# Optimization experiments

Measured on AMD Instinct MI355X. Metric: run time of the kernel, lower is better.

The kernel has to match this reference:

```python
import jax, jax.numpy as jnp
import numpy as np

C = 1024        # number of classes
N = 8           # proxies per class
ALLNUM = C * N  # 8192 total proxies
DIM = 512
R = 0.05
TOPK = int(np.ceil(R * ALLNUM))  # 410
LAM = 0.3
B = 2048


def setup_inputs() -> dict:
    key = jax.random.key(0)
    k1, k2, k3 = jax.random.split(key, 3)
    inp = jax.random.normal(k1, (B, DIM), dtype=jnp.float32)
    target = jax.random.randint(k2, (B,), 0, C, dtype=jnp.int64)
    # kaiming-uniform-initialized proxies approximated by scaled normal init
    proxies = jax.random.normal(k3, (DIM, ALLNUM), dtype=jnp.float32)
    instance_label = jnp.repeat(jnp.arange(C, dtype=jnp.int64), N)  # [ALLNUM]
    return {"input": inp, "target": target, "Proxies": proxies,
            "instance_label": instance_label}


def reference(input, target, Proxies, instance_label):
    # L2-normalize each proxy column (F.normalize along dim=0, eps=1e-12)
    norm = jnp.maximum(jnp.linalg.norm(Proxies, axis=0, keepdims=True), 1e-12)
    centers = Proxies / norm                             # [DIM, ALLNUM]
    similarity = input @ centers                          # [B, ALLNUM]

    positive_mask = (target[:, None] == instance_label[None, :]).astype(similarity.dtype)
    _, indices = jax.lax.top_k(similarity + 1000.0 * positive_mask, TOPK)  # [B, TOPK]

    rows = jnp.arange(similarity.shape[0])[:, None]
    mask = jnp.zeros_like(similarity).at[rows, indices].set(1.0)
    prob_a = mask * similarity                            # sparse-masked similarities

    y_instance_onehot = jax.nn.one_hot(instance_label, C, dtype=similarity.dtype)  # [ALLNUM, C]
    logits = prob_a @ y_instance_onehot                   # [B, C]

    y_target_onehot = jax.nn.one_hot(target, C, dtype=similarity.dtype)  # [B, C]
    logits_mask = 1.0 - (logits == 0.0).astype(similarity.dtype)

    # scale_mask_softmax with scale=1 along dim=1
    e = jnp.exp(logits) * logits_mask
    predict = e / (1e-8 + jnp.sum(e, axis=1, keepdims=True))
    lossClassify = jnp.mean(jnp.sum(-y_target_onehot * jnp.log(predict + 1e-20), axis=1))

    # proxy regularizer: cross-entropy of proxy-vs-class logits
    simCenter = centers.T @ centers                       # [ALLNUM, ALLNUM]
    centers_logits = simCenter @ y_instance_onehot        # [ALLNUM, C]
    logp = jax.nn.log_softmax(centers_logits, axis=1)
    reg = -jnp.mean(jnp.take_along_axis(logp, instance_label[:, None], axis=1))

    return (lossClassify + LAM * reg, lossClassify)
```

## Files before the change

### kernel.cpp

```cpp
#include <hip/hip_runtime.h>
#include <hip/hip_bf16.h>
#include <math.h>

#define C_CLS   1024
#define NPROXY  8
#define ALLNUM  8192
#define DIM     512
#define TOPK    410
#define LAM     0.3f
#define BATCH   2048

#define BAND_CAP_BLK 40
#define ROW_CAP      512
#define GCAP         64

typedef __bf16 bf16x8 __attribute__((ext_vector_type(8)));
typedef float floatx4 __attribute__((ext_vector_type(4)));
typedef unsigned short ushort_t;

#define WS_RNORM 0
#define WS_SIG   8192
#define WS_LP    10240
#define WS_RP    12288
#define WS_CNT   14336
#define WS_NDEF  16384
#define WS_FLAG  18432
#define WS_CLS   20480
#define WS_BVAL  (WS_CLS + 2048*1024)
#define WS_BCOL  (WS_BVAL + 2048*512)
#define WS_ABF   (WS_BCOL + 2048*256)
#define WS_PBF   (WS_ABF + 524288)
#define WS_STBF  (WS_PBF + 2097152)
#define WS_MX    (WS_STBF + 262144)
#define WS_SE    (WS_MX + 65536)
#define WS_DIAG  (WS_SE + 65536)
#define WS_SYNC  (WS_DIAG + 8192)

__device__ inline float block_reduce(float v, int is_max, float* red, int t) {
    #pragma unroll
    for (int o = 32; o > 0; o >>= 1) {
        float w = __shfl_down(v, o);
        v = is_max ? fmaxf(v, w) : (v + w);
    }
    __syncthreads();
    if ((t & 63) == 0) red[t >> 6] = v;
    __syncthreads();
    float r = is_max ? fmaxf(fmaxf(red[0], red[1]), fmaxf(red[2], red[3]))
                     : (red[0] + red[1] + red[2] + red[3]);
    __syncthreads();
    return r;
}

__device__ inline ushort_t f2bf(float f) {
    unsigned u = __float_as_uint(f);
    return (ushort_t)((u + 0x7FFFu + ((u >> 16) & 1u)) >> 16);
}

__device__ inline float bf2f(ushort_t u) {
    return __uint_as_float(((unsigned)u) << 16);
}

__device__ inline void ld_g2l_16(const void* g, void* l) {
    __builtin_amdgcn_global_load_lds(
        (const __attribute__((address_space(1))) unsigned int*)g,
        (__attribute__((address_space(3))) unsigned int*)l,
        16, 0, 0);
}

__device__ inline unsigned f2ord(float f) {
    unsigned u = __float_as_uint(f);
    return (u & 0x80000000u) ? ~u : (u | 0x80000000u);
}

__global__ __launch_bounds__(256) void k_prep1(const float* __restrict__ P,
                                               const float* __restrict__ input,
                                               float* __restrict__ rnorm,
                                               float* __restrict__ rowsig,
                                               ushort_t* __restrict__ Abf,
                                               ushort_t* __restrict__ Pbf,
                                               ushort_t* __restrict__ Stbf,
                                               unsigned* __restrict__ zaux,
                                               unsigned* __restrict__ zsync) {
    __shared__ float stile[512 * 17];
    __shared__ float cred[256];
    __shared__ float s_rn[16];
    int bx = blockIdx.x, t = threadIdx.x;
    if (bx < 512) {
        int c0 = bx * 16;
        #pragma unroll
        for (int it = 0; it < 8; ++it) {
            int r = it * 64 + (t >> 2);
            int c4 = (t & 3) * 4;
            float4 v = *(const float4*)&P[(size_t)r * ALLNUM + c0 + c4];
            stile[r * 17 + c4]     = v.x;
            stile[r * 17 + c4 + 1] = v.y;
            stile[r * 17 + c4 + 2] = v.z;
            stile[r * 17 + c4 + 3] = v.w;
        }
        __syncthreads();
        int tc = t & 15, g = t >> 4;
        float s = 0.f;
        #pragma unroll 8
        for (int k = 0; k < 32; ++k) {
            float v = stile[(g * 32 + k) * 17 + tc];
            s += v * v;
        }
        cred[g * 16 + tc] = s;
        __syncthreads();
        if (g == 0) {
            float tot = 0.f;
            #pragma unroll
            for (int k = 0; k < 16; ++k) tot += cred[k * 16 + tc];
            float r = 1.0f / fmaxf(sqrtf(tot), 1e-12f);
            rnorm[c0 + tc] = r;
            s_rn[tc] = r;
        }
        __syncthreads();
        #pragma unroll
        for (int p = 0; p < 8; ++p) {
            int idx = t + 256 * p;
            int c = idx >> 7, d4 = (idx & 127) * 4;
            ushort4 o;
            o.x = f2bf(stile[(d4    ) * 17 + c]);
            o.y = f2bf(stile[(d4 + 1) * 17 + c]);
            o.z = f2bf(stile[(d4 + 2) * 17 + c]);
            o.w = f2bf(stile[(d4 + 3) * 17 + c]);
            *(ushort4*)&Pbf[(size_t)(c0 + c) * DIM + d4] = o;
        }
        #pragma unroll
        for (int p = 0; p < 2; ++p) {
            int idx = t + 256 * p;
            int cc = idx >> 8, d2 = (idx & 255) * 2;
            float v0 = 0.f, v1 = 0.f;
            #pragma unroll
            for (int n = 0; n < 8; ++n) {
                float rr = s_rn[cc * 8 + n];
                v0 += stile[(d2    ) * 17 + cc * 8 + n] * rr;
                v1 += stile[(d2 + 1) * 17 + cc * 8 + n] * rr;
            }
            ushort2 o; o.x = f2bf(v0); o.y = f2bf(v1);
            *(ushort2*)&Stbf[(size_t)(bx * 2 + cc) * DIM + d2] = o;
        }
    } else if (bx < 512 + 1024) {
        int a = bx - 512;
        int idx = a * 256 + t;
        float4 v = ((const float4*)input)[idx];
        ushort4 o;
        o.x = f2bf(v.x); o.y = f2bf(v.y); o.z = f2bf(v.z); o.w = f2bf(v.w);
        ((ushort4*)Abf)[idx] = o;
        float sq = v.x * v.x + v.y * v.y + v.z * v.z + v.w * v.w;
        #pragma unroll
        for (int off = 32; off > 0; off >>= 1) sq += __shfl_down(sq, off);
        int lane = t & 63, w = t >> 6;
        if (lane == 0) cred[w] = sq;
        __syncthreads();
        if (t == 0) {
            rowsig[2 * a]     = sqrtf(cred[0] + cred[1]);
            rowsig[2 * a + 1] = sqrtf(cred[2] + cred[3]);
        }
    } else {
        for (int i = t; i < 3 * 2048; i += 256) zaux[i] = 0u;
        if (t < 64) zsync[t] = 0u;
    }
}

__global__ __launch_bounds__(512, 2) void k_gemms(const ushort_t* __restrict__ Abf,
                                                  const ushort_t* __restrict__ Pbf,
                                                  const ushort_t* __restrict__ Stbf,
                                                  const float* __restrict__ rnorm,
                                                  const float* __restrict__ rowsig,
                                                  const int* __restrict__ target,
                                                  float* __restrict__ g_cls,
                                                  float* __restrict__ g_bval,
                                                  ushort_t* __restrict__ g_bcol,
                                                  unsigned* __restrict__ g_cnt,
                                                  unsigned* __restrict__ g_ndef,
                                                  unsigned* __restrict__ g_flag,
                                                  float* __restrict__ g_mx,
                                                  float* __restrict__ g_se,
                                                  float* __restrict__ g_diag) {
    __shared__ __align__(16) ushort_t smem[65536];
    int bx = blockIdx.x, t = threadIdx.x;
    int w = t >> 6, lane = t & 63;
    int ml = lane & 15, q4 = lane >> 4;

    int kx = bx & 7, sx = bx >> 3;
    int wid = (sx < 32) ? (kx * 32 + sx) : (256 + kx * 32 + (sx - 32));

    if (wid < 256) {
        int bi = (wid & 7) * 256, bj = (wid >> 3) * 256;
        int wm = w >> 2, wn = w & 3;
        ushort_t* sA0 = smem;
        ushort_t* sB0 = smem + 16384;
        ushort_t* sA1 = smem + 32768;
        ushort_t* sB1 = smem + 49152;

        floatx4 acc[8][4];
        #pragma unroll
        for (int mf = 0; mf < 8; ++mf)
            #pragma unroll
            for (int nf = 0; nf < 4; ++nf)
                acc[mf][nf] = (floatx4){0.f, 0.f, 0.f, 0.f};

        #define STAGE0(sa, sb, k0) do {                                        \
            _Pragma("unroll")                                                  \
            for (int it = 0; it < 4; ++it) {                                   \
                int c = w * 256 + it * 64 + lane;                              \
                int m = c >> 3, s = c & 7, qq = s ^ (m & 7);                   \
                ld_g2l_16(Abf + ((size_t)(bi + m) << 9) + (k0) + qq * 8,       \
                          &(sa)[c * 8]);                                       \
            }                                                                  \
            _Pragma("unroll")                                                  \
            for (int it = 0; it < 4; ++it) {                                   \
                int c = w * 256 + it * 64 + lane;                              \
                int m = c >> 3, s = c & 7, qq = s ^ (m & 7);                   \
                ld_g2l_16(Pbf + ((size_t)(bj + m) << 9) + (k0) + qq * 8,       \
                          &(sb)[c * 8]);                                       \
            }                                                                  \
        } while (0)

        STAGE0(sA0, sB0, 0);
        __syncthreads();
        #pragma unroll
        for (int tt = 0; tt < 8; ++tt) {
            ushort_t* cA = (tt & 1) ? sA1 : sA0;
            ushort_t* cB = (tt & 1) ? sB1 : sB0;
            if (tt < 7) {
                if (tt & 1) STAGE0(sA0, sB0, (tt + 1) * 64);
                else        STAGE0(sA1, sB1, (tt + 1) * 64);
            }
            #pragma unroll
            for (int kk = 0; kk < 2; ++kk) {
                bf16x8 bfr[4];
                #pragma unroll
                for (int nf = 0; nf < 4; ++nf) {
                    int n = wn * 64 + nf * 16 + ml;
                    int s = (kk * 4 + q4) ^ (n & 7);
                    bfr[nf] = *(const bf16x8*)&cB[n * 64 + s * 8];
                }
                #pragma unroll
                for (int mf = 0; mf < 8; ++mf) {
                    int m = wm * 128 + mf * 16 + ml;
                    int s = (kk * 4 + q4) ^ (m & 7);
                    bf16x8 af = *(const bf16x8*)&cA[m * 64 + s * 8];
                    #pragma unroll
                    for (int nf = 0; nf < 4; ++nf)
                        acc[mf][nf] = __builtin_amdgcn_mfma_f32_16x16x32_bf16(
                            af, bfr[nf], acc[mf][nf], 0, 0, 0);
                }
            }
            __syncthreads();
        }
        #undef STAGE0

        unsigned char* sb8 = (unsigned char*)smem;
        float*    e_cls = (float*)sb8;
        float*    e_bv  = (float*)(sb8 + 32768);
        ushort_t* e_bc  = (ushort_t*)(sb8 + 73728);
        unsigned* e_cnt = (unsigned*)(sb8 + 94208);
        unsigned* e_nd  = (unsigned*)(sb8 + 95232);

        #pragma unroll
        for (int i = t; i < 8192; i += 512) e_cls[i] = 0.f;
        if (t < 256) { e_cnt[t] = 0u; e_nd[t] = 0u; }
        __syncthreads();

        #pragma unroll
        for (int mf = 0; mf < 8; ++mf) {
            int rl0 = wm * 128 + mf * 16 + q4 * 4;
            int rowb = bi + rl0;
            float4 rs4 = *(const float4*)&rowsig[rowb];
            int4   tg4 = *(const int4*)&target[rowb];
            #pragma unroll
            for (int nf = 0; nf < 4; ++nf) {
                int cl = wn * 64 + nf * 16 + ml;
                int col = bj + cl;
                float sc = rnorm[col];
                int cls = col >> 3;
                int clsl = cl >> 3;
                #pragma unroll
                for (int i = 0; i < 4; ++i) {
                    int rl = rl0 + i;
                    float v = acc[mf][nf][i] * sc;
                    float sg = ((const float*)&rs4)[i] * (1.0f / 22.616f);
                    float hiT = 1.80f * sg, loT = 1.47f * sg;
                    int tg = ((const int*)&tg4)[i];
                    if (cls == tg) {
                        atomicAdd(&e_cls[rl * 32 + clsl], v);
                    } else if (v >= hiT) {
                        atomicAdd(&e_cls[rl * 32 + clsl], v);
                        atomicAdd(&e_nd[rl], 1u);
                    } else if (v >= loT) {
                        unsigned u = atomicAdd(&e_cnt[rl], 1u);
                        if (u < BAND_CAP_BLK) {
                            e_bv[rl * BAND_CAP_BLK + u] = v;
                            e_bc[rl * BAND_CAP_BLK + u] = (ushort_t)col;
                        }
                    }
                }
            }
        }
        __syncthreads();

        int bjc = bj >> 3;
        #pragma unroll
        for (int i = t; i < 8192; i += 512) {
            int rl = i >> 5, c = i & 31;
            g_cls[(size_t)(bi + rl) * C_CLS + bjc + c] = e_cls[i];
        }
        if (t < 256) {
            int row = bi + t;
            unsigned cbb = e_cnt[t];
            unsigned nd = e_nd[t];
            if (nd) atomicAdd(&g_ndef[row], nd);
            if (cbb) {
                unsigned cc = (cbb > BAND_CAP_BLK) ? BAND_CAP_BLK : cbb;
                unsigned base = atomicAdd(&g_cnt[row], cc);
                if (cbb > BAND_CAP_BLK || base + cc > ROW_CAP) g_flag[row] = 1u;
                for (unsigned j = 0; j < cc; ++j) {
                    if (base + j >= ROW_CAP) break;
                    g_bval[(size_t)row * ROW_CAP + base + j] = e_bv[t * BAND_CAP_BLK + j];
                    g_bcol[(size_t)row * ROW_CAP + base + j] = e_bc[t * BAND_CAP_BLK + j];
                }
            }
        }
    } else {
        int id = wid - 256;
        int bi = (id >> 3) * 256, bj = (id & 7) * 128;
        int wm = w >> 1, wn = w & 1;
        ushort_t* sA0 = smem;
        ushort_t* sB0 = smem + 16384;
        ushort_t* sA1 = smem + 32768;
        ushort_t* sB1 = smem + 49152;

        floatx4 acc[4][4];
        #pragma unroll
        for (int mf = 0; mf < 4; ++mf)
            #pragma unroll
            for (int nf = 0; nf < 4; ++nf)
                acc[mf][nf] = (floatx4){0.f, 0.f, 0.f, 0.f};

        #define STAGE1(sa, sb, k0) do {                                        \
            _Pragma("unroll")                                                  \
            for (int it = 0; it < 4; ++it) {                                   \
                int c = w * 256 + it * 64 + lane;                              \
                int m = c >> 3, s = c & 7, qq = s ^ (m & 7);                   \
                ld_g2l_16(Pbf + ((size_t)(bi + m) << 9) + (k0) + qq * 8,       \
                          &(sa)[c * 8]);                                       \
            }                                                                  \
            _Pragma("unroll")                                                  \
            for (int it = 0; it < 2; ++it) {                                   \
                int c = w * 128 + it * 64 + lane;                              \
                int m = c >> 3, s = c & 7, qq = s ^ (m & 7);                   \
                ld_g2l_16(Stbf + ((size_t)(bj + m) << 9) + (k0) + qq * 8,      \
                          &(sb)[c * 8]);                                       \
            }                                                                  \
        } while (0)

        STAGE1(sA0, sB0, 0);
        __syncthreads();
        #pragma unroll
        for (int tt = 0; tt < 8; ++tt) {
            ushort_t* cA = (tt & 1) ? sA1 : sA0;
            ushort_t* cB = (tt & 1) ? sB1 : sB0;
            if (tt < 7) {
                if (tt & 1) STAGE1(sA0, sB0, (tt + 1) * 64);
                else        STAGE1(sA1, sB1, (tt + 1) * 64);
            }
            #pragma unroll
            for (int kk = 0; kk < 2; ++kk) {
                bf16x8 bfr[4];
                #pragma unroll
                for (int nf = 0; nf < 4; ++nf) {
                    int n = wn * 64 + nf * 16 + ml;
                    int s = (kk * 4 + q4) ^ (n & 7);
                    bfr[nf] = *(const bf16x8*)&cB[n * 64 + s * 8];
                }
                #pragma unroll
                for (int mf = 0; mf < 4; ++mf) {
                    int m = wm * 64 + mf * 16 + ml;
                    int s = (kk * 4 + q4) ^ (m & 7);
                    bf16x8 af = *(const bf16x8*)&cA[m * 64 + s * 8];
                    #pragma unroll
                    for (int nf = 0; nf < 4; ++nf)
                        acc[mf][nf] = __builtin_amdgcn_mfma_f32_16x16x32_bf16(
                            af, bfr[nf], acc[mf][nf], 0, 0, 0);
                }
            }
            __syncthreads();
        }
        #undef STAGE1

        int cj = bj >> 7;
        float mloc[4][4], sloc[4][4];
        #pragma unroll
        for (int mf = 0; mf < 4; ++mf) {
            int rowb = bi + wm * 64 + mf * 16 + q4 * 4;
            float4 rnr = *(const float4*)&rnorm[rowb];
            #pragma unroll
            for (int i = 0; i < 4; ++i) {
                float mm = -1e30f;
                #pragma unroll
                for (int nf = 0; nf < 4; ++nf)
                    mm = fmaxf(mm, acc[mf][nf][i] * ((const float*)&rnr)[i]);
                mloc[mf][i] = mm;
            }
        }
        #pragma unroll
        for (int off = 1; off < 16; off <<= 1)
            #pragma unroll
            for (int mf = 0; mf < 4; ++mf)
                #pragma unroll
                for (int i = 0; i < 4; ++i)
                    mloc[mf][i] = fmaxf(mloc[mf][i], __shfl_xor(mloc[mf][i], off));
        #pragma unroll
        for (int mf = 0; mf < 4; ++mf) {
            int rowb = bi + wm * 64 + mf * 16 + q4 * 4;
            float4 rnr = *(const float4*)&rnorm[rowb];
            #pragma unroll
            for (int i = 0; i < 4; ++i) {
                float ss = 0.f;
                int row = rowb + i;
                #pragma unroll
                for (int nf = 0; nf < 4; ++nf) {
                    float v = acc[mf][nf][i] * ((const float*)&rnr)[i];
                    ss += expf(v - mloc[mf][i]);
                    int col = bj + wn * 64 + nf * 16 + ml;
                    if (col == (row >> 3)) g_diag[row] = v;
                }
                sloc[mf][i] = ss;
            }
        }
        #pragma unroll
        for (int off = 1; off < 16; off <<= 1)
            #pragma unroll
            for (int mf = 0; mf < 4; ++mf)
                #pragma unroll
                for (int i = 0; i < 4; ++i)
                    sloc[mf][i] += __shfl_xor(sloc[mf][i], off);
        float* s_m = (float*)smem;
        float* s_s = s_m + 512;
        if (ml == 0) {
            #pragma unroll
            for (int mf = 0; mf < 4; ++mf)
                #pragma unroll
                for (int i = 0; i < 4; ++i) {
                    int r = wm * 64 + mf * 16 + q4 * 4 + i;
                    s_m[r * 2 + wn] = mloc[mf][i];
                    s_s[r * 2 + wn] = sloc[mf][i];
                }
        }
        __syncthreads();
        if (t < 256) {
            float m0 = s_m[2 * t], m1 = s_m[2 * t + 1];
            float s0 = s_s[2 * t], s1 = s_s[2 * t + 1];
            float M = fmaxf(m0, m1);
            float S = s0 * expf(m0 - M) + s1 * expf(m1 - M);
            g_mx[(size_t)(bi + t) * 8 + cj] = M;
            g_se[(size_t)(bi + t) * 8 + cj] = S;
        }
    }
}

__device__ inline void suffix_select1(unsigned* s_hist, unsigned kk,
                                      unsigned* s_wtot, unsigned* sh_bin,
                                      unsigned* sh_k, int t, int lane, int wid) {
    unsigned h = s_hist[t];
    unsigned v = h;
    #pragma unroll
    for (int off = 1; off < 64; off <<= 1) {
        unsigned o = __shfl_down(v, off);
        if (lane + off < 64) v += o;
    }
    if (lane == 0) s_wtot[wid] = v;
    __syncthreads();
    unsigned above = v - h;
    for (int w2 = wid + 1; w2 < 4; ++w2) above += s_wtot[w2];
    unsigned cum = above + h;
    if (cum >= kk && above < kk) { *sh_bin = (unsigned)t; *sh_k = kk - above; }
    __syncthreads();
}

__global__ __launch_bounds__(256) void k_finish(const int* __restrict__ target,
                                                const float* __restrict__ rowsig,
                                                const float* __restrict__ rnorm,
                                                const ushort_t* __restrict__ Abf,
                                                const ushort_t* __restrict__ Pbf,
                                                const float* __restrict__ g_cls,
                                                const float* __restrict__ g_bval,
                                                const ushort_t* __restrict__ g_bcol,
                                                const unsigned* __restrict__ g_cnt,
                                                const unsigned* __restrict__ g_ndef,
                                                const unsigned* __restrict__ g_flag,
                                                float* __restrict__ loss_part,
                                                const float* __restrict__ g_mx,
                                                const float* __restrict__ g_se,
                                                const float* __restrict__ g_diag,
                                                float* __restrict__ reg_part,
                                                unsigned* __restrict__ sync,
                                                float* __restrict__ out) {
    __shared__ __align__(16) unsigned char smem[16384];
    __shared__ unsigned s_last;
    int bx = blockIdx.x, t = threadIdx.x;
    int lane = t & 63, wid = t >> 6;

    if (bx < 2048) {
        float*    s_cls  = (float*)smem;
        float*    s_bval = (float*)(smem + 4096);
        ushort_t* s_bcol = (ushort_t*)(smem + 6144);
        unsigned* s_hist = (unsigned*)(smem + 7168);
        float*    s_arow = (float*)(smem + 8192);
        unsigned* s_wtot = (unsigned*)(smem + 10240);
        unsigned* shv    = (unsigned*)(smem + 10256);
        float*    shf    = (float*)(smem + 10272);
        float*    red    = (float*)(smem + 10288);
        float*    s_gval = (float*)(smem + 10304);

        int b = bx;
        int tgt = target[b];
        float sig = rowsig[b] * (1.0f / 22.616f);
        float hiT = 1.80f * sig, loT = 1.47f * sig;
        float binscale = 256.0f / (hiT - loT);

        ((float4*)s_cls)[t] = ((const float4*)(g_cls + (size_t)b * C_CLS))[t];
        unsigned cnt = g_cnt[b], nd = g_ndef[b], fl = g_flag[b];
        int kq = (TOPK - NPROXY) - (int)nd;
        int ok = (fl == 0u) && (cnt <= ROW_CAP) && (kq >= 0) && ((int)cnt >= kq);
        if (t == 0) shv[0] = 0u;
        s_hist[t] = 0u;
        __syncthreads();

        if (ok) {
            if (kq > 0) {
                for (int j = t; j < (int)cnt; j += 256) {
                    float v = g_bval[(size_t)b * ROW_CAP + j];
                    s_bval[j] = v;
                    s_bcol[j] = g_bcol[(size_t)b * ROW_CAP + j];
                    int bin = (int)((v - loT) * binscale);
                    bin = (bin > 255) ? 255 : bin;
                    atomicAdd(&s_hist[bin], 1u);
                }
                __syncthreads();
                suffix_select1(s_hist, (unsigned)kq, s_wtot, &shv[1], &shv[2], t, lane, wid);
                int Bb = (int)shv[1];
                int knew = (int)shv[2];
                for (int j = t; j < (int)cnt; j += 256) {
                    float v = s_bval[j];
                    int bin = (int)((v - loT) * binscale);
                    bin = (bin > 255) ? 255 : bin;
                    if (bin == Bb) {
                        unsigned g = atomicAdd(&shv[0], 1u);
                        if (g < GCAP) s_gval[g] = v;
                    }
                }
                __syncthreads();
                int gc = (int)shv[0];
                if (gc <= GCAP) {
                    if (t < gc) {
                        float vj = s_gval[t];
                        unsigned g = 0, geq = 0;
                        for (int i = 0; i < gc; ++i) {
                            float vi = s_gval[i];
                            g   += (vi > vj) ? 1u : 0u;
                            geq += (vi >= vj) ? 1u : 0u;
                        }
                        if (g < (unsigned)knew && geq >= (unsigned)knew) shf[0] = vj;
                    }
                } else {
                    for (int j = t; j < (int)cnt; j += 256) {
                        float vj = s_bval[j];
                        unsigned g = 0, geq = 0;
                        for (int i = 0; i < (int)cnt; ++i) {
                            float vi = s_bval[i];
                            g   += (vi > vj) ? 1u : 0u;
                            geq += (vi >= vj) ? 1u : 0u;
                        }
                        if (g < (unsigned)kq && geq >= (unsigned)kq) shf[0] = vj;
                    }
                }
                __syncthreads();
                float thr = shf[0];
                for (int j = t; j < (int)cnt; j += 256)
                    if (s_bval[j] >= thr)
                        atomicAdd(&s_cls[s_bcol[j] >> 3], s_bval[j]);
            }
        } else {
            for (int i = t; i < DIM; i += 256)
                s_arow[i] = bf2f(Abf[(size_t)b * DIM + i]);
            #pragma unroll
            for (int i = 0; i < 4; ++i) s_cls[t + 256 * i] = 0.f;
            __syncthreads();
            float4 v4[8];
            for (int p = 0; p < 8; ++p) {
                int f = t + 256 * p;
                float vv[4];
                for (int e = 0; e < 4; ++e) {
                    int col = 4 * f + e;
                    const ushort_t* pc = Pbf + (size_t)col * DIM;
                    float a = 0.f;
                    for (int d = 0; d < DIM; ++d)
                        a += s_arow[d] * bf2f(pc[d]);
                    vv[e] = a * rnorm[col];
                }
                float4 o; o.x = vv[0]; o.y = vv[1]; o.z = vv[2]; o.w = vv[3];
                v4[p] = o;
            }
            #pragma unroll
            for (int p = 0; p < 8; ++p) {
                int f = t + 256 * p;
                const float* pv = (const float*)&v4[p];
                if ((f >> 1) == tgt)
                    atomicAdd(&s_cls[tgt], pv[0] + pv[1] + pv[2] + pv[3]);
            }
            unsigned L = 0u, R = 0xFFFFFFFFu;
            for (int it = 0; it < 33 && R - L > 1; ++it) {
                unsigned mid = L + ((R - L) >> 1);
                float c = 0.f;
                #pragma unroll
                for (int p = 0; p < 8; ++p) {
                    int f = t + 256 * p;
                    const float* pv = (const float*)&v4[p];
                    if ((f >> 1) != tgt) {
                        #pragma unroll
                        for (int e = 0; e < 4; ++e)
                            c += (f2ord(pv[e]) >= mid) ? 1.f : 0.f;
                    }
                }
                c = block_reduce(c, 0, red, t);
                if (c >= (float)(TOPK - NPROXY)) L = mid; else R = mid;
                __syncthreads();
            }
            #pragma unroll
            for (int p = 0; p < 8; ++p) {
                int f = t + 256 * p;
                const float* pv = (const float*)&v4[p];
                if ((f >> 1) != tgt) {
                    #pragma unroll
                    for (int e = 0; e < 4; ++e)
                        if (f2ord(pv[e]) >= L)
                            atomicAdd(&s_cls[f >> 1], pv[e]);
                }
            }
        }
        __syncthreads();

        float4 cv = ((const float4*)s_cls)[t];
        float m = -1e30f;
        if (cv.x != 0.0f) m = fmaxf(m, cv.x);
        if (cv.y != 0.0f) m = fmaxf(m, cv.y);
        if (cv.z != 0.0f) m = fmaxf(m, cv.z);
        if (cv.w != 0.0f) m = fmaxf(m, cv.w);
        m = block_reduce(m, 1, red, t);
        float se = 0.f;
        if (cv.x != 0.0f) se += expf(cv.x - m);
        if (cv.y != 0.0f) se += expf(cv.y - m);
        if (cv.z != 0.0f) se += expf(cv.z - m);
        if (cv.w != 0.0f) se += expf(cv.w - m);
        se = block_reduce(se, 0, red, t);
        if (t == 0) {
            float lt = s_cls[tgt];
            float predict_t = expf(lt - m) / (1e-8f * expf(-m) + se);
            loss_part[b] = -logf(predict_t + 1e-20f);
        }
    } else {
        float* red2 = (float*)smem;
        int rb = bx - 2048;
        float val = 0.f;
        if (t < 64) {
            int row = rb * 64 + t;
            float mj[8], sj[8];
            float M = -1e30f;
            #pragma unroll
            for (int j = 0; j < 8; ++j) {
                mj[j] = g_mx[(size_t)row * 8 + j];
                sj[j] = g_se[(size_t)row * 8 + j];
                M = fmaxf(M, mj[j]);
            }
            float S = 0.f;
            #pragma unroll
            for (int j = 0; j < 8; ++j) S += sj[j] * expf(mj[j] - M);
            val = M + logf(S) - g_diag[row];
        }
        val = block_reduce(val, 0, red2, t);
        if (t == 0) reg_part[rb] = val;
    }

    if (t == 0) {
        __threadfence();
        unsigned old = atomicAdd(&sync[0], 1u);
        s_last = (old == 2175u) ? 1u : 0u;
    }
    __syncthreads();
    if (s_last) {
        __threadfence();
        float* red = (float*)smem;
        float4 a = ((const float4*)loss_part)[t];
        float4 b2 = ((const float4*)loss_part)[t + 256];
        float ls = a.x + a.y + a.z + a.w + b2.x + b2.y + b2.z + b2.w;
        float rs = 0.f;
        if (t < 32) {
            float4 c = ((const float4*)reg_part)[t];
            rs = c.x + c.y + c.z + c.w;
        }
        ls = block_reduce(ls, 0, red, t);
        rs = block_reduce(rs, 0, red, t);
        if (t == 0) {
            float lc = ls / (float)BATCH;
            float rg = rs / (float)ALLNUM;
            out[0] = lc + LAM * rg;
            out[1] = lc;
        }
    }
}

extern "C" void kernel_launch(void* const* d_in, const int* in_sizes, int n_in,
                              void* d_out, int out_size, void* d_ws, size_t ws_size,
                              hipStream_t stream) {
    const float* input  = (const float*)d_in[0];
    const int*   target = (const int*)d_in[1];
    const float* P      = (const float*)d_in[2];

    float* ws        = (float*)d_ws;
    float* rnorm     = ws + WS_RNORM;
    float* rowsig    = ws + WS_SIG;
    float* loss_part = ws + WS_LP;
    float* reg_part  = ws + WS_RP;
    unsigned* g_cnt  = (unsigned*)(ws + WS_CNT);
    unsigned* g_ndef = (unsigned*)(ws + WS_NDEF);
    unsigned* g_flag = (unsigned*)(ws + WS_FLAG);
    float* g_cls     = ws + WS_CLS;
    float* g_bval    = ws + WS_BVAL;
    ushort_t* g_bcol = (ushort_t*)(ws + WS_BCOL);
    ushort_t* Abf    = (ushort_t*)(ws + WS_ABF);
    ushort_t* Pbf    = (ushort_t*)(ws + WS_PBF);
    ushort_t* Stbf   = (ushort_t*)(ws + WS_STBF);
    float* g_mx      = ws + WS_MX;
    float* g_se      = ws + WS_SE;
    float* g_diag    = ws + WS_DIAG;
    unsigned* syncp  = (unsigned*)(ws + WS_SYNC);
    float* out       = (float*)d_out;

    hipLaunchKernelGGL(k_prep1, dim3(512 + 1024 + 1), dim3(256), 0, stream,
                       P, input, rnorm, rowsig, Abf, Pbf, Stbf, g_cnt, syncp);
    hipLaunchKernelGGL(k_gemms, dim3(512), dim3(512), 0, stream,
                       Abf, Pbf, Stbf, rnorm, rowsig, target,
                       g_cls, g_bval, g_bcol, g_cnt, g_ndef, g_flag,
                       g_mx, g_se, g_diag);
    hipLaunchKernelGGL(k_finish, dim3(2048 + 128), dim3(256), 0, stream,
                       target, rowsig, rnorm, Abf, Pbf,
                       g_cls, g_bval, g_bcol, g_cnt, g_ndef, g_flag,
                       loss_part, g_mx, g_se, g_diag, reg_part, syncp, out);
}
```

Before: 184.4 us.

## Split proxy prep into norm/class-sum blocks and separate 32x32 transpose blocks

Restructures the prep kernel: proxy column norms and per-class summed centers are computed by 256 blocks reading P directly from global memory, while the bf16 transpose of P into Pbf moves to 4096 small blocks using a 32x32 padded shared tile. This replaces 512 blocks that each staged a 512x16 column slab in large shared memory. The aim is higher occupancy and more parallelism in prep, at the cost of reading P from global memory twice and more, smaller blocks.

```diff
diff --git a/kernel.cpp b/kernel.cpp
--- a/kernel.cpp
+++ b/kernel.cpp
@@ -81,68 +81,45 @@
                                                ushort_t* __restrict__ Stbf,
                                                unsigned* __restrict__ zaux,
                                                unsigned* __restrict__ zsync) {
-    __shared__ float stile[512 * 17];
-    __shared__ float cred[256];
-    __shared__ float s_rn[16];
+    __shared__ float tile[32][33];
+    __shared__ float s_rn[32];
+    float* cred = &tile[0][0];
     int bx = blockIdx.x, t = threadIdx.x;
-    if (bx < 512) {
-        int c0 = bx * 16;
-        #pragma unroll
-        for (int it = 0; it < 8; ++it) {
-            int r = it * 64 + (t >> 2);
-            int c4 = (t & 3) * 4;
-            float4 v = *(const float4*)&P[(size_t)r * ALLNUM + c0 + c4];
-            stile[r * 17 + c4]     = v.x;
-            stile[r * 17 + c4 + 1] = v.y;
-            stile[r * 17 + c4 + 2] = v.z;
-            stile[r * 17 + c4 + 3] = v.w;
-        }
-        __syncthreads();
-        int tc = t & 15, g = t >> 4;
+    if (bx < 256) {
+        int tc = t & 31, g = t >> 5;
+        int c = bx * 32 + tc;
+        const float* pc = P + (size_t)(g * 64) * ALLNUM + c;
         float s = 0.f;
         #pragma unroll 8
-        for (int k = 0; k < 32; ++k) {
-            float v = stile[(g * 32 + k) * 17 + tc];
+        for (int d = 0; d < 64; ++d) {
+            float v = pc[(size_t)d * ALLNUM];
             s += v * v;
         }
-        cred[g * 16 + tc] = s;
+        cred[g * 32 + tc] = s;
         __syncthreads();
         if (g == 0) {
             float tot = 0.f;
             #pragma unroll
-            for (int k = 0; k < 16; ++k) tot += cred[k * 16 + tc];
+            for (int k = 0; k < 8; ++k) tot += cred[k * 32 + tc];
             float r = 1.0f / fmaxf(sqrtf(tot), 1e-12f);
-            rnorm[c0 + tc] = r;
+            rnorm[c] = r;
             s_rn[tc] = r;
         }
         __syncthreads();
         #pragma unroll
         for (int p = 0; p < 8; ++p) {
             int idx = t + 256 * p;
-            int c = idx >> 7, d4 = (idx & 127) * 4;
-            ushort4 o;
-            o.x = f2bf(stile[(d4    ) * 17 + c]);
-            o.y = f2bf(stile[(d4 + 1) * 17 + c]);
-            o.z = f2bf(stile[(d4 + 2) * 17 + c]);
-            o.w = f2bf(stile[(d4 + 3) * 17 + c]);
-            *(ushort4*)&Pbf[(size_t)(c0 + c) * DIM + d4] = o;
-        }
-        #pragma unroll
-        for (int p = 0; p < 2; ++p) {
-            int idx = t + 256 * p;
-            int cc = idx >> 8, d2 = (idx & 255) * 2;
-            float v0 = 0.f, v1 = 0.f;
-            #pragma unroll
-            for (int n = 0; n < 8; ++n) {
-                float rr = s_rn[cc * 8 + n];
-                v0 += stile[(d2    ) * 17 + cc * 8 + n] * rr;
-                v1 += stile[(d2 + 1) * 17 + cc * 8 + n] * rr;
-            }
-            ushort2 o; o.x = f2bf(v0); o.y = f2bf(v1);
-            *(ushort2*)&Stbf[(size_t)(bx * 2 + cc) * DIM + d2] = o;
-        }
-    } else if (bx < 512 + 1024) {
-        int a = bx - 512;
+            int d = idx >> 2, cc = idx & 3;
+            const float* pp = P + (size_t)d * ALLNUM + bx * 32 + cc * 8;
+            const float* rr = &s_rn[cc * 8];
+            float4 a = *(const float4*)pp;
+            float4 b = *(const float4*)(pp + 4);
+            float v = a.x * rr[0] + a.y * rr[1] + a.z * rr[2] + a.w * rr[3] +
+                      b.x * rr[4] + b.y * rr[5] + b.z * rr[6] + b.w * rr[7];
+            Stbf[(size_t)(bx * 4 + cc) * DIM + d] = f2bf(v);
+        }
+    } else if (bx < 256 + 1024) {
+        int a = bx - 256;
         int idx = a * 256 + t;
         float4 v = ((const float4*)input)[idx];
         ushort4 o;
@@ -157,6 +134,19 @@
         if (t == 0) {
             rowsig[2 * a]     = sqrtf(cred[0] + cred[1]);
             rowsig[2 * a + 1] = sqrtf(cred[2] + cred[3]);
+        }
+    } else if (bx < 256 + 1024 + 4096) {
+        int id = bx - 1280;
+        int c0 = (id & 255) * 32, r0 = (id >> 8) * 32;
+        int tc = t & 31, tr = t >> 5;
+        #pragma unroll
+        for (int p = 0; p < 4; ++p)
+            tile[tr + p * 8][tc] = P[(size_t)(r0 + tr + p * 8) * ALLNUM + c0 + tc];
+        __syncthreads();
+        #pragma unroll
+        for (int p = 0; p < 4; ++p) {
+            int oc = tr + p * 8;
+            Pbf[(size_t)(c0 + oc) * DIM + r0 + tc] = f2bf(tile[tc][oc]);
         }
     } else {
         for (int i = t; i < 3 * 2048; i += 256) zaux[i] = 0u;
@@ -740,7 +730,7 @@
     unsigned* syncp  = (unsigned*)(ws + WS_SYNC);
     float* out       = (float*)d_out;
 
-    hipLaunchKernelGGL(k_prep1, dim3(512 + 1024 + 1), dim3(256), 0, stream,
+    hipLaunchKernelGGL(k_prep1, dim3(256 + 1024 + 4096 + 1), dim3(256), 0, stream,
                        P, input, rnorm, rowsig, Abf, Pbf, Stbf, g_cnt, syncp);
     hipLaunchKernelGGL(k_gemms, dim3(512), dim3(512), 0, stream,
                        Abf, Pbf, Stbf, rnorm, rowsig, target,
```

Measured after the change: 182.9 us. About the same (-0.8%).
